# Kernel tuning notes

Hardware: AMD Instinct MI355X
Metric: run time of the kernel (lower is better)

Reference implementation:

```python
import jax, jax.numpy as jnp
import numpy as np

N = 50000      # nodes
E = 800000     # edges (avg degree 16)
F_IN = 128     # input feature dim
HID = 64       # hidden_channels
HEADS = 4
OUT = 64       # out_channels


def _gatv2_layer(x, src, dst, Wl, Wr, att, bias, heads, ch, n):
    # lin_l (source) and lin_r (target) projections -> [N, H, C]
    xl = (x @ Wl).reshape(n, heads, ch)
    xr = (x @ Wr).reshape(n, heads, ch)
    # per-edge GATv2 attention logits: a^T LeakyReLU(xl_j + xr_i)
    e = jax.nn.leaky_relu(xl[src] + xr[dst], negative_slope=0.2)  # [E, H, C]
    score = jnp.einsum('ehc,hc->eh', e, att)                      # [E, H]
    # segment softmax over incoming edges of each destination node
    m = jax.ops.segment_max(score, dst, num_segments=n)           # [N, H]
    m = jnp.where(jnp.isfinite(m), m, 0.0)
    p = jnp.exp(score - m[dst])
    denom = jax.ops.segment_sum(p, dst, num_segments=n)           # [N, H]
    alpha = p / (denom[dst] + 1e-16)                              # [E, H]
    # weighted scatter-aggregate of source messages xl_j
    out = jax.ops.segment_sum(alpha[..., None] * xl[src], dst, num_segments=n)
    return out.reshape(n, heads * ch) + bias


def setup_inputs() -> dict:
    key = jax.random.key(0)
    ks = jax.random.split(key, 16)

    def w(k, shape, fan_in):
        return (jax.random.normal(k, shape, dtype=jnp.float32) / np.sqrt(fan_in)).astype(jnp.float32)

    return {
        'x': jax.random.normal(ks[0], (N, F_IN), dtype=jnp.float32),
        'Wl1': w(ks[1], (F_IN, HEADS * HID), F_IN),
        'Wr1': w(ks[2], (F_IN, HEADS * HID), F_IN),
        'att1': w(ks[3], (HEADS, HID), HID),
        'b1': jnp.zeros((HEADS * HID,), jnp.float32),
        'Wl2': w(ks[4], (HEADS * HID, HEADS * HID), HEADS * HID),
        'Wr2': w(ks[5], (HEADS * HID, HEADS * HID), HEADS * HID),
        'att2': w(ks[6], (HEADS, HID), HID),
        'b2': jnp.zeros((HEADS * HID,), jnp.float32),
        'Wl3': w(ks[7], (HEADS * HID, OUT), HEADS * HID),
        'Wr3': w(ks[8], (HEADS * HID, OUT), HEADS * HID),
        'att3': w(ks[9], (1, OUT), OUT),
        'b3': jnp.zeros((OUT,), jnp.float32),
        'Wlin': w(ks[10], (OUT, HID), OUT),
        'blin': jnp.zeros((HID,), jnp.float32),
        'edge_index': jax.random.randint(ks[11], (2, E), 0, N, dtype=jnp.int64
                                         if jax.config.read('jax_enable_x64') else jnp.int32),
    }


def reference(x, Wl1, Wr1, att1, b1, Wl2, Wr2, att2, b2, Wl3, Wr3, att3, b3, Wlin, blin, edge_index):
    src, dst = edge_index[0], edge_index[1]
    h = jax.nn.elu(_gatv2_layer(x, src, dst, Wl1, Wr1, att1, b1, HEADS, HID, N))
    h = jax.nn.elu(_gatv2_layer(h, src, dst, Wl2, Wr2, att2, b2, HEADS, HID, N))
    h = _gatv2_layer(h, src, dst, Wl3, Wr3, att3, b3, 1, OUT, N)
    # F.dropout(p=0.5, training=False) -> identity in eval mode
    return h @ Wlin + blin
```

## Files before the change

### kernel.cpp

```cpp
#include <hip/hip_runtime.h>
#include <hip/hip_fp16.h>

#define NN 50000
#define EE 800000

typedef float f32x4 __attribute__((ext_vector_type(4)));
typedef _Float16 f16x8 __attribute__((ext_vector_type(8)));
typedef _Float16 f16x4 __attribute__((ext_vector_type(4)));
typedef _Float16 f16x2 __attribute__((ext_vector_type(2)));

__global__ void hist_kernel(const int* __restrict__ dst, int* __restrict__ counts, int E) {
    int idx = blockIdx.x * blockDim.x + threadIdx.x;
    int stride = gridDim.x * blockDim.x;
    for (int e = idx; e < E; e += stride)
        atomicAdd(&counts[dst[e]], 1);
}

__global__ void scan_phaseA(const int* __restrict__ counts, int* __restrict__ bsum, int n) {
    __shared__ int buf[256];
    int b = blockIdx.x, t = threadIdx.x;
    int i = b * 256 + t;
    buf[t] = (i < n) ? counts[i] : 0;
    __syncthreads();
#pragma unroll
    for (int off = 128; off; off >>= 1) {
        if (t < off) buf[t] += buf[t + off];
        __syncthreads();
    }
    if (t == 0) bsum[b] = buf[0];
}

__global__ void scan_phaseB(int* __restrict__ bsum, int* __restrict__ row_off_n, int nb) {
    __shared__ int buf[256];
    int t = threadIdx.x;
    int v = (t < nb) ? bsum[t] : 0;
    buf[t] = v;
    __syncthreads();
#pragma unroll
    for (int off = 1; off < 256; off <<= 1) {
        int x = (t >= off) ? buf[t - off] : 0;
        __syncthreads();
        buf[t] += x;
        __syncthreads();
    }
    if (t < nb) bsum[t] = buf[t] - v;
    if (t == 255) *row_off_n = buf[255];
}

__global__ void scan_phaseC(const int* __restrict__ counts, const int* __restrict__ bsum,
                            int* __restrict__ row_off, int n) {
    __shared__ int buf[256];
    int b = blockIdx.x, t = threadIdx.x;
    int i = b * 256 + t;
    int v = (i < n) ? counts[i] : 0;
    buf[t] = v;
    __syncthreads();
#pragma unroll
    for (int off = 1; off < 256; off <<= 1) {
        int x = (t >= off) ? buf[t - off] : 0;
        __syncthreads();
        buf[t] += x;
        __syncthreads();
    }
    if (i < n) row_off[i] = bsum[b] + buf[t] - v;
}

__global__ void scatter_kernel(const int* __restrict__ src, const int* __restrict__ dst,
                               const int* __restrict__ row_off, int* __restrict__ cursor,
                               int* __restrict__ esrc, int E) {
    int idx = blockIdx.x * blockDim.x + threadIdx.x;
    int stride = gridDim.x * blockDim.x;
    for (int e = idx; e < E; e += stride) {
        int d = dst[e];
        int pos = row_off[d] + atomicAdd(&cursor[d], 1);
        esrc[pos] = src[e];
    }
}

__device__ __forceinline__ void wfrag_store(__half* o, int K, int col, int k, float v) {
    int KS = K >> 5;
    int cgni = col >> 4, l15 = col & 15;
    int ks = k >> 5, qq = (k >> 3) & 3, ee = k & 7;
    size_t flat = ((size_t)(cgni * KS + ks) * 64 + qq * 16 + l15) * 8 + ee;
    o[flat] = __float2half_rn(v);
}

__global__ void prep_all(const float* __restrict__ Wl1, const float* __restrict__ Wr1,
                         const float* __restrict__ Wl2, const float* __restrict__ Wr2,
                         const float* __restrict__ Wl3, const float* __restrict__ Wr3,
                         const float* __restrict__ Wlin,
                         __half* __restrict__ w1, __half* __restrict__ w2,
                         __half* __restrict__ w3, __half* __restrict__ w4,
                         const float* __restrict__ x, __half* __restrict__ xf, int n4x) {
    int idx = blockIdx.x * blockDim.x + threadIdx.x;
    if (idx < 233472) {
        const float* W; __half* o; int K, Nc, roff, li;
        if (idx < 65536) {
            K = 128; Nc = 256; o = w1;
            if (idx < 32768) { W = Wl1; li = idx; roff = 0; }
            else             { W = Wr1; li = idx - 32768; roff = 256; }
        } else if (idx < 196608) {
            K = 256; Nc = 256; o = w2;
            if (idx < 131072) { W = Wl2; li = idx - 65536; roff = 0; }
            else              { W = Wr2; li = idx - 131072; roff = 256; }
        } else if (idx < 229376) {
            K = 256; Nc = 64; o = w3;
            if (idx < 212992) { W = Wl3; li = idx - 196608; roff = 0; }
            else              { W = Wr3; li = idx - 212992; roff = 64; }
        } else {
            K = 64; Nc = 64; o = w4; W = Wlin; li = idx - 229376; roff = 0;
        }
        int k = li / Nc, n = li - k * Nc;
        wfrag_store(o, K, roff + n, k, W[li]);
    } else {
        int xi = idx - 233472;
        if (xi < n4x) {
            float4 v = *(const float4*)(x + (size_t)xi * 4);
            f16x4 h = {(_Float16)v.x, (_Float16)v.y, (_Float16)v.z, (_Float16)v.w};
            *(f16x4*)((_Float16*)xf + (size_t)xi * 4) = h;
        }
    }
}

template <int KS, int COLG>
__global__ __launch_bounds__(COLG * 256) void gemm_ws(
        const __half* __restrict__ A, const __half* __restrict__ Bt,
        int M, int nTiles, int Nc, int splitCol,
        __half* __restrict__ outL, __half* __restrict__ outR,
        float* __restrict__ outF, const float* __restrict__ bias) {
    constexpr int K = KS * 32;
    int tid = threadIdx.x;
    int lane = tid & 63;
    int w = tid >> 6;
    int rs = w & 3;
    int cg = w >> 2;
    int l15 = lane & 15, q = lane >> 4;
    int colbase = blockIdx.y * (COLG * 64) + cg * 64;

    const _Float16* Ap = (const _Float16*)A;
    const f16x8* Bf = (const f16x8*)Bt;
    int cgni0 = (blockIdx.y * COLG + cg) * 4;

    f16x8 bfrag[KS][4];
#pragma unroll
    for (int ks = 0; ks < KS; ++ks)
#pragma unroll
        for (int ni = 0; ni < 4; ++ni)
            bfrag[ks][ni] = Bf[((size_t)(cgni0 + ni) * KS + ks) * 64 + lane];

    int tile = blockIdx.x;
    if (tile >= nTiles) return;

    f16x8 afrag[KS];
    {
        int row = tile * 64 + rs * 16 + l15;
        if (row >= M) row = M - 1;
        const _Float16* ap = Ap + (size_t)row * K + q * 8;
#pragma unroll
        for (int ks = 0; ks < KS; ++ks) afrag[ks] = *(const f16x8*)(ap + ks * 32);
    }

    while (true) {
        int next = tile + gridDim.x;
        bool has = (next < nTiles);
        f16x8 anext[KS];
        if (has) {
            int row = next * 64 + rs * 16 + l15;
            if (row >= M) row = M - 1;
            const _Float16* ap = Ap + (size_t)row * K + q * 8;
#pragma unroll
            for (int ks = 0; ks < KS; ++ks) anext[ks] = *(const f16x8*)(ap + ks * 32);
        }

        f32x4 acc[4] = {};
#pragma unroll
        for (int ks = 0; ks < KS; ++ks)
#pragma unroll
            for (int ni = 0; ni < 4; ++ni)
                acc[ni] = __builtin_amdgcn_mfma_f32_16x16x32_f16(afrag[ks], bfrag[ks][ni], acc[ni], 0, 0, 0);

#pragma unroll
        for (int ni = 0; ni < 4; ++ni) {
            int gc = colbase + ni * 16 + l15;
            if (outF) {
                float bv = bias ? bias[gc] : 0.f;
#pragma unroll
                for (int r = 0; r < 4; ++r) {
                    int gr = tile * 64 + rs * 16 + q * 4 + r;
                    if (gr < M) outF[(size_t)gr * Nc + gc] = acc[ni][r] + bv;
                }
            } else {
                __half* dp = outL; int cc = gc;
                if (gc >= splitCol) { dp = outR; cc = gc - splitCol; }
#pragma unroll
                for (int r = 0; r < 4; ++r) {
                    int gr = tile * 64 + rs * 16 + q * 4 + r;
                    if (gr < M) dp[(size_t)gr * splitCol + cc] = __float2half_rn(acc[ni][r]);
                }
            }
        }
        if (!has) break;
#pragma unroll
        for (int ks = 0; ks < KS; ++ks) afrag[ks] = anext[ks];
        tile = next;
    }
}

template <int CTRL>
__device__ __forceinline__ float dpp_add_f32(float x) {
    int y = __builtin_amdgcn_mov_dpp(__float_as_int(x), CTRL, 0xF, 0xF, true);
    return x + __int_as_float(y);
}

__global__ __launch_bounds__(256, 8) void gat_gather_h4(
        const __half* __restrict__ xl, const __half* __restrict__ xr,
        const float* __restrict__ att, const float* __restrict__ bias,
        const int* __restrict__ row_off, const int* __restrict__ esrc,
        __half* __restrict__ out, int n) {
    const float LOG2E = 1.44269504f;
    int wave = threadIdx.x >> 6;
    int lane = threadIdx.x & 63;
    int node = blockIdx.x * 4 + wave;
    if (node >= n) return;
    int slot = lane >> 5;
    unsigned jj = lane & 31;

    const uint4* xl16 = (const uint4*)xl;

    f16x2 xrv[4];
    *(uint4*)(&xrv[0]) = ((const uint4*)xr)[((unsigned)node << 5) + jj];

    float4 a0 = *(const float4*)(att + jj * 8);
    float4 a1 = *(const float4*)(att + jj * 8 + 4);
    f16x2 atv[4] = {
        {(_Float16)(a0.x * LOG2E), (_Float16)(a0.y * LOG2E)},
        {(_Float16)(a0.z * LOG2E), (_Float16)(a0.w * LOG2E)},
        {(_Float16)(a1.x * LOG2E), (_Float16)(a1.y * LOG2E)},
        {(_Float16)(a1.z * LOG2E), (_Float16)(a1.w * LOG2E)}};
    const f16x2 k02 = {(_Float16)0.2f, (_Float16)0.2f};

    float acc[8] = {};
    float L = 0.f;

    int e0 = row_off[node], e1 = row_off[node + 1];
    int elast = (e1 > e0) ? e1 - 1 : 0;

    int sA = esrc[min(e0 + 0 + slot, elast)];
    int sB = esrc[min(e0 + 2 + slot, elast)];
    int sC = esrc[min(e0 + 4 + slot, elast)];
    int sD = esrc[min(e0 + 6 + slot, elast)];
    uint4 A = xl16[((unsigned)sA << 5) + jj];
    uint4 B = xl16[((unsigned)sB << 5) + jj];
    uint4 C = xl16[((unsigned)sC << 5) + jj];
    uint4 D = xl16[((unsigned)sD << 5) + jj];

#define H4_PHASE(BUF, EB)                                                     \
    {                                                                         \
        f16x2 v[4];                                                           \
        *(uint4*)(&v[0]) = BUF;                                               \
        float t = 0.f;                                                        \
        _Pragma("unroll")                                                     \
        for (int k = 0; k < 4; ++k) {                                         \
            f16x2 s = v[k] + xrv[k];                                          \
            f16x2 r = __builtin_elementwise_max(s, s * k02);                  \
            t = __builtin_amdgcn_fdot2(r, atv[k], t, false);                  \
        }                                                                     \
        t = dpp_add_f32<0xB1>(t);                                             \
        t = dpp_add_f32<0x4E>(t);                                             \
        t = dpp_add_f32<0x141>(t);                                            \
        float p = exp2f(t);                                                   \
        p = ((EB) + slot < e1) ? p : 0.f;                                     \
        L += p;                                                               \
        _Pragma("unroll")                                                     \
        for (int k = 0; k < 4; ++k) {                                         \
            acc[2 * k]     = fmaf((float)v[k].x, p, acc[2 * k]);              \
            acc[2 * k + 1] = fmaf((float)v[k].y, p, acc[2 * k + 1]);          \
        }                                                                     \
    }

    {
        int e = e0;
        while (true) {
            int ns = esrc[min(e + 8 + slot, elast)];
            H4_PHASE(A, e)
            A = xl16[((unsigned)ns << 5) + jj];
            e += 2; if (e >= e1) break;
            ns = esrc[min(e + 8 + slot, elast)];
            H4_PHASE(B, e)
            B = xl16[((unsigned)ns << 5) + jj];
            e += 2; if (e >= e1) break;
            ns = esrc[min(e + 8 + slot, elast)];
            H4_PHASE(C, e)
            C = xl16[((unsigned)ns << 5) + jj];
            e += 2; if (e >= e1) break;
            ns = esrc[min(e + 8 + slot, elast)];
            H4_PHASE(D, e)
            D = xl16[((unsigned)ns << 5) + jj];
            e += 2; if (e >= e1) break;
        }
    }
#undef H4_PHASE

#pragma unroll
    for (int k = 0; k < 8; ++k) acc[k] += __shfl_xor(acc[k], 32);
    L += __shfl_xor(L, 32);

    if (slot == 0) {
        float inv = 1.f / (L + 1e-16f);
        float4 b0 = *(const float4*)(bias + jj * 8);
        float4 b1v = *(const float4*)(bias + jj * 8 + 4);
        float bb[8] = {b0.x, b0.y, b0.z, b0.w, b1v.x, b1v.y, b1v.z, b1v.w};
        f16x8 o0;
#pragma unroll
        for (int k = 0; k < 8; ++k) {
            float vA = acc[k] * inv + bb[k];
            vA = vA > 0.f ? vA : __expf(vA) - 1.f;
            o0[k] = (_Float16)vA;
        }
        *(f16x8*)((_Float16*)out + ((size_t)node << 8) + jj * 8) = o0;
    }
}

__global__ __launch_bounds__(256, 8) void gat_gather_h1(
        const __half* __restrict__ xl, const __half* __restrict__ xr,
        const float* __restrict__ att, const float* __restrict__ bias,
        const int* __restrict__ row_off, const int* __restrict__ esrc,
        __half* __restrict__ out, int n) {
    const float LOG2E = 1.44269504f;
    int wave = threadIdx.x >> 6;
    int lane = threadIdx.x & 63;
    int node = blockIdx.x * 4 + wave;
    if (node >= n) return;
    int eslot = lane >> 3;
    unsigned j = lane & 7;

    const uint4* xl16 = (const uint4*)xl;

    f16x2 xrv[4];
    *(uint4*)(&xrv[0]) = ((const uint4*)xr)[((unsigned)node << 3) + j];

    float4 a0 = *(const float4*)(att + j * 8);
    float4 a1 = *(const float4*)(att + j * 8 + 4);
    f16x2 atv[4] = {
        {(_Float16)(a0.x * LOG2E), (_Float16)(a0.y * LOG2E)},
        {(_Float16)(a0.z * LOG2E), (_Float16)(a0.w * LOG2E)},
        {(_Float16)(a1.x * LOG2E), (_Float16)(a1.y * LOG2E)},
        {(_Float16)(a1.z * LOG2E), (_Float16)(a1.w * LOG2E)}};
    const f16x2 k02 = {(_Float16)0.2f, (_Float16)0.2f};

    float acc[8] = {};
    float L = 0.f;

    int e0 = row_off[node], e1 = row_off[node + 1];
    int elast = (e1 > e0) ? e1 - 1 : 0;

    int sA = esrc[min(e0 +  0 + eslot, elast)];
    int sB = esrc[min(e0 +  8 + eslot, elast)];
    int sC = esrc[min(e0 + 16 + eslot, elast)];
    uint4 A = xl16[((unsigned)sA << 3) + j];
    uint4 B = xl16[((unsigned)sB << 3) + j];
    uint4 C = xl16[((unsigned)sC << 3) + j];

#define H1_PHASE(R, EB)                                                       \
    {                                                                         \
        f16x2 v[4];                                                           \
        *(uint4*)(&v[0]) = R;                                                 \
        float t0 = 0.f, t1 = 0.f;                                             \
        {                                                                     \
            f16x2 s0 = v[0] + xrv[0];                                         \
            f16x2 r0 = __builtin_elementwise_max(s0, s0 * k02);               \
            t0 = __builtin_amdgcn_fdot2(r0, atv[0], t0, false);               \
            f16x2 s1 = v[1] + xrv[1];                                         \
            f16x2 r1 = __builtin_elementwise_max(s1, s1 * k02);               \
            t0 = __builtin_amdgcn_fdot2(r1, atv[1], t0, false);               \
            f16x2 s2 = v[2] + xrv[2];                                         \
            f16x2 r2 = __builtin_elementwise_max(s2, s2 * k02);               \
            t1 = __builtin_amdgcn_fdot2(r2, atv[2], t1, false);               \
            f16x2 s3 = v[3] + xrv[3];                                         \
            f16x2 r3 = __builtin_elementwise_max(s3, s3 * k02);               \
            t1 = __builtin_amdgcn_fdot2(r3, atv[3], t1, false);               \
        }                                                                     \
        float t = t0 + t1;                                                    \
        t = dpp_add_f32<0xB1>(t);                                             \
        t = dpp_add_f32<0x4E>(t);                                             \
        t = dpp_add_f32<0x141>(t);                                            \
        float p = exp2f(t);                                                   \
        p = ((EB) + eslot < e1) ? p : 0.f;                                    \
        L += p;                                                               \
        _Pragma("unroll")                                                     \
        for (int k = 0; k < 4; ++k) {                                         \
            acc[2 * k]     = fmaf((float)v[k].x, p, acc[2 * k]);              \
            acc[2 * k + 1] = fmaf((float)v[k].y, p, acc[2 * k + 1]);          \
        }                                                                     \
    }

    {
        int e = e0;
        while (true) {
            int ns = esrc[min(e + 24 + eslot, elast)];
            H1_PHASE(A, e)
            A = xl16[((unsigned)ns << 3) + j];
            e += 8; if (e >= e1) break;
            ns = esrc[min(e + 24 + eslot, elast)];
            H1_PHASE(B, e)
            B = xl16[((unsigned)ns << 3) + j];
            e += 8; if (e >= e1) break;
            ns = esrc[min(e + 24 + eslot, elast)];
            H1_PHASE(C, e)
            C = xl16[((unsigned)ns << 3) + j];
            e += 8; if (e >= e1) break;
        }
    }
#undef H1_PHASE

#pragma unroll
    for (int k = 0; k < 8; ++k) {
        acc[k] += __shfl_xor(acc[k], 8);
        acc[k] += __shfl_xor(acc[k], 16);
        acc[k] += __shfl_xor(acc[k], 32);
    }
    L += __shfl_xor(L, 8);
    L += __shfl_xor(L, 16);
    L += __shfl_xor(L, 32);

    if (eslot == 0) {
        float inv = 1.f / (L + 1e-16f);
        float4 b0 = *(const float4*)(bias + j * 8);
        float4 b1v = *(const float4*)(bias + j * 8 + 4);
        float bb[8] = {b0.x, b0.y, b0.z, b0.w, b1v.x, b1v.y, b1v.z, b1v.w};
        f16x8 ov;
#pragma unroll
        for (int k = 0; k < 8; ++k)
            ov[k] = (_Float16)(acc[k] * inv + bb[k]);
        *(f16x8*)((_Float16*)out + ((size_t)node << 6) + j * 8) = ov;
    }
}

extern "C" void kernel_launch(void* const* d_in, const int* in_sizes, int n_in,
                              void* d_out, int out_size, void* d_ws, size_t ws_size,
                              hipStream_t stream) {
    const float* x    = (const float*)d_in[0];
    const float* Wl1  = (const float*)d_in[1];
    const float* Wr1  = (const float*)d_in[2];
    const float* att1 = (const float*)d_in[3];
    const float* b1   = (const float*)d_in[4];
    const float* Wl2  = (const float*)d_in[5];
    const float* Wr2  = (const float*)d_in[6];
    const float* att2 = (const float*)d_in[7];
    const float* b2   = (const float*)d_in[8];
    const float* Wl3  = (const float*)d_in[9];
    const float* Wr3  = (const float*)d_in[10];
    const float* att3 = (const float*)d_in[11];
    const float* b3   = (const float*)d_in[12];
    const float* Wlin = (const float*)d_in[13];
    const float* blin = (const float*)d_in[14];
    const int*   ei   = (const int*)d_in[15];
    const int* src = ei;
    const int* dst = ei + EE;

    const int N = NN, E = EE;
    const int NB = (N + 255) / 256;

    __half* xf = (__half*)d_ws;
    __half* xl = xf + (size_t)N * 128;
    __half* xr = xl + (size_t)N * 256;
    __half* H  = xr + (size_t)N * 256;
    __half* G  = H + (size_t)N * 256;
    __half* w1 = G + (size_t)N * 64;
    __half* w2 = w1 + 65536;
    __half* w3 = w2 + 131072;
    __half* w4 = w3 + 32768;
    int* row_off = (int*)(w4 + 4096);
    int* tmp     = row_off + (N + 1);
    int* esrc    = tmp + 2 * N;
    int* bsum    = esrc + E;

    hipMemsetAsync(tmp, 0, (size_t)2 * N * sizeof(int), stream);
    hist_kernel<<<1024, 256, 0, stream>>>(dst, tmp, E);
    scan_phaseA<<<NB, 256, 0, stream>>>(tmp, bsum, N);
    scan_phaseB<<<1, 256, 0, stream>>>(bsum, row_off + N, NB);
    scan_phaseC<<<NB, 256, 0, stream>>>(tmp, bsum, row_off, N);
    scatter_kernel<<<1024, 256, 0, stream>>>(src, dst, row_off, tmp + N, esrc, E);

    int n4x = N * 128 / 4;
    prep_all<<<(233472 + n4x + 255) / 256, 256, 0, stream>>>(
        Wl1, Wr1, Wl2, Wr2, Wl3, Wr3, Wlin, w1, w2, w3, w4, x, xf, n4x);

    int nTiles = (N + 63) / 64;
    int gatherBlocks = (N + 3) / 4;

    gemm_ws<4, 2><<<dim3(128, 4), 512, 0, stream>>>(
        xf, w1, N, nTiles, 512, 256, xl, xr, nullptr, nullptr);
    gat_gather_h4<<<gatherBlocks, 256, 0, stream>>>(xl, xr, att1, b1, row_off, esrc, H, N);

    gemm_ws<8, 2><<<dim3(128, 4), 512, 0, stream>>>(
        H, w2, N, nTiles, 512, 256, xl, xr, nullptr, nullptr);
    gat_gather_h4<<<gatherBlocks, 256, 0, stream>>>(xl, xr, att2, b2, row_off, esrc, H, N);

    gemm_ws<8, 2><<<dim3(256, 1), 512, 0, stream>>>(
        H, w3, N, nTiles, 128, 64, xl, xr, nullptr, nullptr);
    gat_gather_h1<<<gatherBlocks, 256, 0, stream>>>(xl, xr, att3, b3, row_off, esrc, G, N);

    gemm_ws<2, 1><<<dim3(512, 1), 256, 0, stream>>>(
        G, w4, N, nTiles, 64, 64, nullptr, nullptr, (float*)d_out, blin);
}
```

Baseline: 463.1 us.

## Use persistent atomic work-stealing gather kernels, remap GEMM block order, fast exp2

New measurement: 948.1 us. 105% more time.

```diff
diff --git a/kernel.cpp b/kernel.cpp
--- a/kernel.cpp
+++ b/kernel.cpp
@@ -122,7 +122,7 @@
     }
 }
 
-template <int KS, int COLG>
+template <int KS, int COLG, int NBX>
 __global__ __launch_bounds__(COLG * 256) void gemm_ws(
         const __half* __restrict__ A, const __half* __restrict__ Bt,
         int M, int nTiles, int Nc, int splitCol,
@@ -135,11 +135,22 @@
     int rs = w & 3;
     int cg = w >> 2;
     int l15 = lane & 15, q = lane >> 4;
-    int colbase = blockIdx.y * (COLG * 64) + cg * 64;
+
+    int bx, by;
+    if constexpr (NBX > 0) {
+        int bid = blockIdx.x;
+        by = (bid >> 3) & 3;
+        bx = ((bid >> 5) << 3) | (bid & 7);
+    } else {
+        bx = blockIdx.x; by = blockIdx.y;
+    }
+    const int gstride = (NBX > 0) ? NBX : gridDim.x;
+
+    int colbase = by * (COLG * 64) + cg * 64;
 
     const _Float16* Ap = (const _Float16*)A;
     const f16x8* Bf = (const f16x8*)Bt;
-    int cgni0 = (blockIdx.y * COLG + cg) * 4;
+    int cgni0 = (by * COLG + cg) * 4;
 
     f16x8 bfrag[KS][4];
 #pragma unroll
@@ -148,7 +159,7 @@
         for (int ni = 0; ni < 4; ++ni)
             bfrag[ks][ni] = Bf[((size_t)(cgni0 + ni) * KS + ks) * 64 + lane];
 
-    int tile = blockIdx.x;
+    int tile = bx;
     if (tile >= nTiles) return;
 
     f16x8 afrag[KS];
@@ -161,7 +172,7 @@
     }
 
     while (true) {
-        int next = tile + gridDim.x;
+        int next = tile + gstride;
         bool has = (next < nTiles);
         f16x8 anext[KS];
         if (has) {
@@ -212,23 +223,26 @@
     return x + __int_as_float(y);
 }
 
+__device__ __forceinline__ float fast_exp2(float x) {
+    float r;
+    asm("v_exp_f32 %0, %1\n\ts_nop 0" : "=v"(r) : "v"(x));
+    return r;
+}
+
 __global__ __launch_bounds__(256, 8) void gat_gather_h4(
         const __half* __restrict__ xl, const __half* __restrict__ xr,
         const float* __restrict__ att, const float* __restrict__ bias,
         const int* __restrict__ row_off, const int* __restrict__ esrc,
-        __half* __restrict__ out, int n) {
+        __half* __restrict__ out, int n, int* __restrict__ counter) {
     const float LOG2E = 1.44269504f;
     int wave = threadIdx.x >> 6;
     int lane = threadIdx.x & 63;
-    int node = blockIdx.x * 4 + wave;
-    if (node >= n) return;
+    int gw = blockIdx.x * 4 + wave;
     int slot = lane >> 5;
     unsigned jj = lane & 31;
 
     const uint4* xl16 = (const uint4*)xl;
-
-    f16x2 xrv[4];
-    *(uint4*)(&xrv[0]) = ((const uint4*)xr)[((unsigned)node << 5) + jj];
+    const uint4* xr16 = (const uint4*)xr;
 
     float4 a0 = *(const float4*)(att + jj * 8);
     float4 a1 = *(const float4*)(att + jj * 8 + 4);
@@ -238,86 +252,104 @@
         {(_Float16)(a1.x * LOG2E), (_Float16)(a1.y * LOG2E)},
         {(_Float16)(a1.z * LOG2E), (_Float16)(a1.w * LOG2E)}};
     const f16x2 k02 = {(_Float16)0.2f, (_Float16)0.2f};
-
-    float acc[8] = {};
-    float L = 0.f;
-
-    int e0 = row_off[node], e1 = row_off[node + 1];
-    int elast = (e1 > e0) ? e1 - 1 : 0;
-
-    int sA = esrc[min(e0 + 0 + slot, elast)];
-    int sB = esrc[min(e0 + 2 + slot, elast)];
-    int sC = esrc[min(e0 + 4 + slot, elast)];
-    int sD = esrc[min(e0 + 6 + slot, elast)];
-    uint4 A = xl16[((unsigned)sA << 5) + jj];
-    uint4 B = xl16[((unsigned)sB << 5) + jj];
-    uint4 C = xl16[((unsigned)sC << 5) + jj];
-    uint4 D = xl16[((unsigned)sD << 5) + jj];
+    float4 bv0 = *(const float4*)(bias + jj * 8);
+    float4 bv1 = *(const float4*)(bias + jj * 8 + 4);
+
+    auto process = [&](int node) {
+        f16x2 xrv[4];
+        *(uint4*)(&xrv[0]) = xr16[((unsigned)node << 5) + jj];
+
+        float acc[8] = {};
+        float L = 0.f;
+
+        int e0 = row_off[node], e1 = row_off[node + 1];
+        int elast = (e1 > e0) ? e1 - 1 : 0;
+
+        int sA = esrc[min(e0 + 0 + slot, elast)];
+        int sB = esrc[min(e0 + 2 + slot, elast)];
+        int sC = esrc[min(e0 + 4 + slot, elast)];
+        int sD = esrc[min(e0 + 6 + slot, elast)];
+        uint4 A = xl16[((unsigned)sA << 5) + jj];
+        uint4 B = xl16[((unsigned)sB << 5) + jj];
+        uint4 C = xl16[((unsigned)sC << 5) + jj];
+        uint4 D = xl16[((unsigned)sD << 5) + jj];
 
 #define H4_PHASE(BUF, EB)                                                     \
-    {                                                                         \
-        f16x2 v[4];                                                           \
-        *(uint4*)(&v[0]) = BUF;                                               \
-        float t = 0.f;                                                        \
-        _Pragma("unroll")                                                     \
-        for (int k = 0; k < 4; ++k) {                                         \
-            f16x2 s = v[k] + xrv[k];                                          \
-            f16x2 r = __builtin_elementwise_max(s, s * k02);                  \
-            t = __builtin_amdgcn_fdot2(r, atv[k], t, false);                  \
-        }                                                                     \
-        t = dpp_add_f32<0xB1>(t);                                             \
-        t = dpp_add_f32<0x4E>(t);                                             \
-        t = dpp_add_f32<0x141>(t);                                            \
-        float p = exp2f(t);                                                   \
-        p = ((EB) + slot < e1) ? p : 0.f;                                     \
-        L += p;                                                               \
-        _Pragma("unroll")                                                     \
-        for (int k = 0; k < 4; ++k) {                                         \
-            acc[2 * k]     = fmaf((float)v[k].x, p, acc[2 * k]);              \
-            acc[2 * k + 1] = fmaf((float)v[k].y, p, acc[2 * k + 1]);          \
-        }                                                                     \
-    }
-
-    {
-        int e = e0;
-        while (true) {
-            int ns = esrc[min(e + 8 + slot, elast)];
-            H4_PHASE(A, e)
-            A = xl16[((unsigned)ns << 5) + jj];
-            e += 2; if (e >= e1) break;
-            ns = esrc[min(e + 8 + slot, elast)];
-            H4_PHASE(B, e)
-            B = xl16[((unsigned)ns << 5) + jj];
-            e += 2; if (e >= e1) break;
-            ns = esrc[min(e + 8 + slot, elast)];
-            H4_PHASE(C, e)
-            C = xl16[((unsigned)ns << 5) + jj];
-            e += 2; if (e >= e1) break;
-            ns = esrc[min(e + 8 + slot, elast)];
-            H4_PHASE(D, e)
-            D = xl16[((unsigned)ns << 5) + jj];
-            e += 2; if (e >= e1) break;
-        }
-    }
+        {                                                                     \
+            f16x2 v[4];                                                       \
+            *(uint4*)(&v[0]) = BUF;                                           \
+            float t = 0.f;                                                    \
+            _Pragma("unroll")                                                 \
+            for (int k = 0; k < 4; ++k) {                                     \
+                f16x2 s = v[k] + xrv[k];                                      \
+                f16x2 r = __builtin_elementwise_max(s, s * k02);              \
+                t = __builtin_amdgcn_fdot2(r, atv[k], t, false);              \
+            }                                                                 \
+            t = dpp_add_f32<0xB1>(t);                                         \
+            t = dpp_add_f32<0x4E>(t);                                         \
+            t = dpp_add_f32<0x141>(t);                                        \
+            float p = fast_exp2(t);                                           \
+            p = ((EB) + slot < e1) ? p : 0.f;                                 \
+            L += p;                                                           \
+            _Pragma("unroll")                                                 \
+            for (int k = 0; k < 4; ++k) {                                     \
+                acc[2 * k]     = fmaf((float)v[k].x, p, acc[2 * k]);          \
+                acc[2 * k + 1] = fmaf((float)v[k].y, p, acc[2 * k + 1]);      \
+            }                                                                 \
+        }
+
+        {
+            int e = e0;
+            while (true) {
+                int ns = esrc[min(e + 8 + slot, elast)];
+                H4_PHASE(A, e)
+                A = xl16[((unsigned)ns << 5) + jj];
+                e += 2; if (e >= e1) break;
+                ns = esrc[min(e + 8 + slot, elast)];
+                H4_PHASE(B, e)
+                B = xl16[((unsigned)ns << 5) + jj];
+                e += 2; if (e >= e1) break;
+                ns = esrc[min(e + 8 + slot, elast)];
+                H4_PHASE(C, e)
+                C = xl16[((unsigned)ns << 5) + jj];
+                e += 2; if (e >= e1) break;
+                ns = esrc[min(e + 8 + slot, elast)];
+                H4_PHASE(D, e)
+                D = xl16[((unsigned)ns << 5) + jj];
+                e += 2; if (e >= e1) break;
+            }
+        }
 #undef H4_PHASE
 
 #pragma unroll
-    for (int k = 0; k < 8; ++k) acc[k] += __shfl_xor(acc[k], 32);
-    L += __shfl_xor(L, 32);
-
-    if (slot == 0) {
-        float inv = 1.f / (L + 1e-16f);
-        float4 b0 = *(const float4*)(bias + jj * 8);
-        float4 b1v = *(const float4*)(bias + jj * 8 + 4);
-        float bb[8] = {b0.x, b0.y, b0.z, b0.w, b1v.x, b1v.y, b1v.z, b1v.w};
-        f16x8 o0;
-#pragma unroll
-        for (int k = 0; k < 8; ++k) {
-            float vA = acc[k] * inv + bb[k];
-            vA = vA > 0.f ? vA : __expf(vA) - 1.f;
-            o0[k] = (_Float16)vA;
-        }
-        *(f16x8*)((_Float16*)out + ((size_t)node << 8) + jj * 8) = o0;
+        for (int k = 0; k < 8; ++k) acc[k] += __shfl_xor(acc[k], 32);
+        L += __shfl_xor(L, 32);
+
+        if (slot == 0) {
+            float inv = 1.f / (L + 1e-16f);
+            float bb[8] = {bv0.x, bv0.y, bv0.z, bv0.w, bv1.x, bv1.y, bv1.z, bv1.w};
+            f16x8 o0;
+#pragma unroll
+            for (int k = 0; k < 8; ++k) {
+                float vA = acc[k] * inv + bb[k];
+                vA = vA > 0.f ? vA : __expf(vA) - 1.f;
+                o0[k] = (_Float16)vA;
+            }
+            *(f16x8*)((_Float16*)out + ((size_t)node << 8) + jj * 8) = o0;
+        }
+    };
+
+    process(gw * 2);
+    process(gw * 2 + 1);
+
+    while (true) {
+        int t = 0;
+        if (lane == 0) t = atomicAdd(counter, 4);
+        t = __shfl(t, 0);
+        int base = 16384 + t;
+        if (base >= n) break;
+        int end = min(base + 4, n);
+        for (int node = base; node < end; ++node) process(node);
     }
 }
 
@@ -325,19 +357,16 @@
         const __half* __restrict__ xl, const __half* __restrict__ xr,
         const float* __restrict__ att, const float* __restrict__ bias,
         const int* __restrict__ row_off, const int* __restrict__ esrc,
-        __half* __restrict__ out, int n) {
+        __half* __restrict__ out, int n, int* __restrict__ counter) {
     const float LOG2E = 1.44269504f;
     int wave = threadIdx.x >> 6;
     int lane = threadIdx.x & 63;
-    int node = blockIdx.x * 4 + wave;
-    if (node >= n) return;
+    int gw = blockIdx.x * 4 + wave;
     int eslot = lane >> 3;
     unsigned j = lane & 7;
 
     const uint4* xl16 = (const uint4*)xl;
-
-    f16x2 xrv[4];
-    *(uint4*)(&xrv[0]) = ((const uint4*)xr)[((unsigned)node << 3) + j];
+    const uint4* xr16 = (const uint4*)xr;
 
     float4 a0 = *(const float4*)(att + j * 8);
     float4 a1 = *(const float4*)(att + j * 8 + 4);
@@ -347,92 +376,110 @@
         {(_Float16)(a1.x * LOG2E), (_Float16)(a1.y * LOG2E)},
         {(_Float16)(a1.z * LOG2E), (_Float16)(a1.w * LOG2E)}};
     const f16x2 k02 = {(_Float16)0.2f, (_Float16)0.2f};
-
-    float acc[8] = {};
-    float L = 0.f;
-
-    int e0 = row_off[node], e1 = row_off[node + 1];
-    int elast = (e1 > e0) ? e1 - 1 : 0;
-
-    int sA = esrc[min(e0 +  0 + eslot, elast)];
-    int sB = esrc[min(e0 +  8 + eslot, elast)];
-    int sC = esrc[min(e0 + 16 + eslot, elast)];
-    uint4 A = xl16[((unsigned)sA << 3) + j];
-    uint4 B = xl16[((unsigned)sB << 3) + j];
-    uint4 C = xl16[((unsigned)sC << 3) + j];
+    float4 b0 = *(const float4*)(bias + j * 8);
+    float4 b1v = *(const float4*)(bias + j * 8 + 4);
+
+    auto process = [&](int node) {
+        f16x2 xrv[4];
+        *(uint4*)(&xrv[0]) = xr16[((unsigned)node << 3) + j];
+
+        float acc[8] = {};
+        float L = 0.f;
+
+        int e0 = row_off[node], e1 = row_off[node + 1];
+        int elast = (e1 > e0) ? e1 - 1 : 0;
+
+        int sA = esrc[min(e0 +  0 + eslot, elast)];
+        int sB = esrc[min(e0 +  8 + eslot, elast)];
+        int sC = esrc[min(e0 + 16 + eslot, elast)];
+        uint4 A = xl16[((unsigned)sA << 3) + j];
+        uint4 B = xl16[((unsigned)sB << 3) + j];
+        uint4 C = xl16[((unsigned)sC << 3) + j];
 
 #define H1_PHASE(R, EB)                                                       \
-    {                                                                         \
-        f16x2 v[4];                                                           \
-        *(uint4*)(&v[0]) = R;                                                 \
-        float t0 = 0.f, t1 = 0.f;                                             \
         {                                                                     \
-            f16x2 s0 = v[0] + xrv[0];                                         \
-            f16x2 r0 = __builtin_elementwise_max(s0, s0 * k02);               \
-            t0 = __builtin_amdgcn_fdot2(r0, atv[0], t0, false);               \
-            f16x2 s1 = v[1] + xrv[1];                                         \
-            f16x2 r1 = __builtin_elementwise_max(s1, s1 * k02);               \
-            t0 = __builtin_amdgcn_fdot2(r1, atv[1], t0, false);               \
-            f16x2 s2 = v[2] + xrv[2];                                         \
-            f16x2 r2 = __builtin_elementwise_max(s2, s2 * k02);               \
-            t1 = __builtin_amdgcn_fdot2(r2, atv[2], t1, false);               \
-            f16x2 s3 = v[3] + xrv[3];                                         \
-            f16x2 r3 = __builtin_elementwise_max(s3, s3 * k02);               \
-            t1 = __builtin_amdgcn_fdot2(r3, atv[3], t1, false);               \
-        }                                                                     \
-        float t = t0 + t1;                                                    \
-        t = dpp_add_f32<0xB1>(t);                                             \
-        t = dpp_add_f32<0x4E>(t);                                             \
-        t = dpp_add_f32<0x141>(t);                                            \
-        float p = exp2f(t);                                                   \
-        p = ((EB) + eslot < e1) ? p : 0.f;                                    \
-        L += p;                                                               \
-        _Pragma("unroll")                                                     \
-        for (int k = 0; k < 4; ++k) {                                         \
-            acc[2 * k]     = fmaf((float)v[k].x, p, acc[2 * k]);              \
-            acc[2 * k + 1] = fmaf((float)v[k].y, p, acc[2 * k + 1]);          \
-        }                                                                     \
-    }
-
-    {
-        int e = e0;
-        while (true) {
-            int ns = esrc[min(e + 24 + eslot, elast)];
-            H1_PHASE(A, e)
-            A = xl16[((unsigned)ns << 3) + j];
-            e += 8; if (e >= e1) break;
-            ns = esrc[min(e + 24 + eslot, elast)];
-            H1_PHASE(B, e)
-            B = xl16[((unsigned)ns << 3) + j];
-            e += 8; if (e >= e1) break;
-            ns = esrc[min(e + 24 + eslot, elast)];
-            H1_PHASE(C, e)
-            C = xl16[((unsigned)ns << 3) + j];
-            e += 8; if (e >= e1) break;
-        }
-    }
+            f16x2 v[4];                                                       \
+            *(uint4*)(&v[0]) = R;                                             \
+            float t0 = 0.f, t1 = 0.f;                                         \
+            {                                                                 \
+                f16x2 s0 = v[0] + xrv[0];                                     \
+                f16x2 r0 = __builtin_elementwise_max(s0, s0 * k02);           \
+                t0 = __builtin_amdgcn_fdot2(r0, atv[0], t0, false);           \
+                f16x2 s1 = v[1] + xrv[1];                                     \
+                f16x2 r1 = __builtin_elementwise_max(s1, s1 * k02);           \
+                t0 = __builtin_amdgcn_fdot2(r1, atv[1], t0, false);           \
+                f16x2 s2 = v[2] + xrv[2];                                     \
+                f16x2 r2 = __builtin_elementwise_max(s2, s2 * k02);           \
+                t1 = __builtin_amdgcn_fdot2(r2, atv[2], t1, false);           \
+                f16x2 s3 = v[3] + xrv[3];                                     \
+                f16x2 r3 = __builtin_elementwise_max(s3, s3 * k02);           \
+                t1 = __builtin_amdgcn_fdot2(r3, atv[3], t1, false);           \
+            }                                                                 \
+            float t = t0 + t1;                                                \
+            t = dpp_add_f32<0xB1>(t);                                         \
+            t = dpp_add_f32<0x4E>(t);                                         \
+            t = dpp_add_f32<0x141>(t);                                        \
+            float p = fast_exp2(t);                                           \
+            p = ((EB) + eslot < e1) ? p : 0.f;                                \
+            L += p;                                                           \
+            _Pragma("unroll")                                                 \
+            for (int k = 0; k < 4; ++k) {                                     \
+                acc[2 * k]     = fmaf((float)v[k].x, p, acc[2 * k]);          \
+                acc[2 * k + 1] = fmaf((float)v[k].y, p, acc[2 * k + 1]);      \
+            }                                                                 \
+        }
+
+        {
+            int e = e0;
+            while (true) {
+                int ns = esrc[min(e + 24 + eslot, elast)];
+                H1_PHASE(A, e)
+                A = xl16[((unsigned)ns << 3) + j];
+                e += 8; if (e >= e1) break;
+                ns = esrc[min(e + 24 + eslot, elast)];
+                H1_PHASE(B, e)
+                B = xl16[((unsigned)ns << 3) + j];
+                e += 8; if (e >= e1) break;
+                ns = esrc[min(e + 24 + eslot, elast)];
+                H1_PHASE(C, e)
+                C = xl16[((unsigned)ns << 3) + j];
+                e += 8; if (e >= e1) break;
+            }
+        }
 #undef H1_PHASE
 
 #pragma unroll
-    for (int k = 0; k < 8; ++k) {
-        acc[k] += __shfl_xor(acc[k], 8);
-        acc[k] += __shfl_xor(acc[k], 16);
-        acc[k] += __shfl_xor(acc[k], 32);
-    }
-    L += __shfl_xor(L, 8);
-    L += __shfl_xor(L, 16);
-    L += __shfl_xor(L, 32);
-
-    if (eslot == 0) {
-        float inv = 1.f / (L + 1e-16f);
-        float4 b0 = *(const float4*)(bias + j * 8);
-        float4 b1v = *(const float4*)(bias + j * 8 + 4);
-        float bb[8] = {b0.x, b0.y, b0.z, b0.w, b1v.x, b1v.y, b1v.z, b1v.w};
-        f16x8 ov;
-#pragma unroll
-        for (int k = 0; k < 8; ++k)
-            ov[k] = (_Float16)(acc[k] * inv + bb[k]);
-        *(f16x8*)((_Float16*)out + ((size_t)node << 6) + j * 8) = ov;
+        for (int k = 0; k < 8; ++k) {
+            acc[k] += __shfl_xor(acc[k], 8);
+            acc[k] += __shfl_xor(acc[k], 16);
+            acc[k] += __shfl_xor(acc[k], 32);
+        }
+        L += __shfl_xor(L, 8);
+        L += __shfl_xor(L, 16);
+        L += __shfl_xor(L, 32);
+
+        if (eslot == 0) {
+            float inv = 1.f / (L + 1e-16f);
+            float bb[8] = {b0.x, b0.y, b0.z, b0.w, b1v.x, b1v.y, b1v.z, b1v.w};
+            f16x8 ov;
+#pragma unroll
+            for (int k = 0; k < 8; ++k)
+                ov[k] = (_Float16)(acc[k] * inv + bb[k]);
+            *(f16x8*)((_Float16*)out + ((size_t)node << 6) + j * 8) = ov;
+        }
+    };
+
+    process(gw * 2);
+    process(gw * 2 + 1);
+
+    while (true) {
+        int t = 0;
+        if (lane == 0) t = atomicAdd(counter, 4);
+        t = __shfl(t, 0);
+        int base = 16384 + t;
+        if (base >= n) break;
+        int end = min(base + 4, n);
+        for (int node = base; node < end; ++node) process(node);
     }
 }
 
@@ -474,8 +521,10 @@
     int* tmp     = row_off + (N + 1);
     int* esrc    = tmp + 2 * N;
     int* bsum    = esrc + E;
+    int* counters = bsum + 256;
 
     hipMemsetAsync(tmp, 0, (size_t)2 * N * sizeof(int), stream);
+    hipMemsetAsync(counters, 0, 3 * sizeof(int), stream);
     hist_kernel<<<1024, 256, 0, stream>>>(dst, tmp, E);
     scan_phaseA<<<NB, 256, 0, stream>>>(tmp, bsum, N);
     scan_phaseB<<<1, 256, 0, stream>>>(bsum, row_off + N, NB);
@@ -487,20 +536,19 @@
         Wl1, Wr1, Wl2, Wr2, Wl3, Wr3, Wlin, w1, w2, w3, w4, x, xf, n4x);
 
     int nTiles = (N + 63) / 64;
-    int gatherBlocks = (N + 3) / 4;
-
-    gemm_ws<4, 2><<<dim3(128, 4), 512, 0, stream>>>(
+
+    gemm_ws<4, 2, 128><<<512, 512, 0, stream>>>(
         xf, w1, N, nTiles, 512, 256, xl, xr, nullptr, nullptr);
-    gat_gather_h4<<<gatherBlocks, 256, 0, stream>>>(xl, xr, att1, b1, row_off, esrc, H, N);
-
-    gemm_ws<8, 2><<<dim3(128, 4), 512, 0, stream>>>(
+    gat_gather_h4<<<2048, 256, 0, stream>>>(xl, xr, att1, b1, row_off, esrc, H, N, counters + 0);
+
+    gemm_ws<8, 2, 128><<<512, 512, 0, stream>>>(
         H, w2, N, nTiles, 512, 256, xl, xr, nullptr, nullptr);
-    gat_gather_h4<<<gatherBlocks, 256, 0, stream>>>(xl, xr, att2, b2, row_off, esrc, H, N);
-
-    gemm_ws<8, 2><<<dim3(256, 1), 512, 0, stream>>>(
+    gat_gather_h4<<<2048, 256, 0, stream>>>(xl, xr, att2, b2, row_off, esrc, H, N, counters + 1);
+
+    gemm_ws<8, 2, 0><<<dim3(256, 1), 512, 0, stream>>>(
         H, w3, N, nTiles, 128, 64, xl, xr, nullptr, nullptr);
-    gat_gather_h1<<<gatherBlocks, 256, 0, stream>>>(xl, xr, att3, b3, row_off, esrc, G, N);
-
-    gemm_ws<2, 1><<<dim3(512, 1), 256, 0, stream>>>(
+    gat_gather_h1<<<2048, 256, 0, stream>>>(xl, xr, att3, b3, row_off, esrc, G, N, counters + 2);
+
+    gemm_ws<2, 1, 0><<<dim3(512, 1), 256, 0, stream>>>(
         G, w4, N, nTiles, 64, 64, nullptr, nullptr, (float*)d_out, blin);
 }
```
